# Kernel optimization log

Measured on AMD Instinct MI355X. Metric: run time of the kernel, lower is better.

Reference implementation:

```python
import jax, jax.numpy as jnp
import numpy as np

NUM_GRAPHS = 4096
NODES_PER_GRAPH = 24
EDGES_PER_GRAPH = 48
LG_EDGES_PER_GRAPH = 144
N_ITER = 4
HID = 128
IN_DIM = 70
EDGE_DIM = 6


def seg_softmax(v, seg, num_seg):
    # numerically-stable softmax over segments; v: [E,1]
    m = jax.ops.segment_max(v, seg, num_segments=num_seg)
    e = jnp.exp(v - m[seg])
    s = jax.ops.segment_sum(e, seg, num_segments=num_seg)
    return e / s[seg]


def setup_inputs() -> dict:
    key = jax.random.key(0)
    ks = jax.random.split(key, 20)
    B, NPG, EPG, LPG = NUM_GRAPHS, NODES_PER_GRAPH, EDGES_PER_GRAPH, LG_EDGES_PER_GRAPH
    N, E, LE = B * NPG, B * EPG, B * LPG
    # graph-consistent random connectivity
    goff_n = (jnp.arange(B, dtype=jnp.int32) * NPG)[:, None]
    src = (goff_n + jax.random.randint(ks[0], (B, EPG), 0, NPG)).reshape(-1)
    dst = (goff_n + jax.random.randint(ks[1], (B, EPG), 0, NPG)).reshape(-1)
    edge_index = jnp.stack([src, dst]).astype(jnp.int32)
    goff_e = (jnp.arange(B, dtype=jnp.int32) * EPG)[:, None]
    lsrc = (goff_e + jax.random.randint(ks[2], (B, LPG), 0, EPG)).reshape(-1)
    ldst = (goff_e + jax.random.randint(ks[3], (B, LPG), 0, EPG)).reshape(-1)
    lg_edge_index = jnp.stack([lsrc, ldst]).astype(jnp.int32)
    edge_batch = jnp.repeat(jnp.arange(B, dtype=jnp.int32), EPG)
    s = 0.1
    inp = {
        "x": jax.random.normal(ks[4], (N, IN_DIM), jnp.float32),
        "edge_attr": jax.random.normal(ks[5], (E, EDGE_DIM), jnp.float32),
        "edge_index": edge_index,
        "lg_edge_index": lg_edge_index,
        "edge_batch": edge_batch,
        # params (stored [in, out] so we apply x @ W + b)
        "w_mlp": jax.random.normal(ks[6], (IN_DIM, HID), jnp.float32) * s,
        "b_mlp": jnp.zeros((HID,), jnp.float32),
        "w_u": jax.random.normal(ks[7], (HID, HID), jnp.float32) * s,
        "w_v": jax.random.normal(ks[8], (HID, HID), jnp.float32) * s,
        "w_edge": jax.random.normal(ks[9], (EDGE_DIM, HID), jnp.float32) * s,
        "w_rel": jax.random.normal(ks[10], (HID, 1), jnp.float32) * s,
        "b_rel": jnp.zeros((1,), jnp.float32),
        "w_root": jax.random.normal(ks[11], (HID, 1), jnp.float32) * s,
        "a": jax.random.normal(ks[12], (1, HID, N_ITER), jnp.float32) * s,
        "a_bias": jnp.zeros((1, 1, N_ITER), jnp.float32),
        "w_gout": jax.random.normal(ks[13], (HID, HID), jnp.float32) * s,
        "b_gout": jnp.zeros((HID,), jnp.float32),
        "w_block": jax.random.normal(ks[14], (HID, HID), jnp.float32) * s,
        "b_block": jnp.zeros((HID,), jnp.float32),
    }
    return inp


def reference(x, edge_attr, edge_index, lg_edge_index, edge_batch,
              w_mlp, b_mlp, w_u, w_v, w_edge, w_rel, b_rel, w_root,
              a, a_bias, w_gout, b_gout, w_block, b_block):
    N = x.shape[0]
    src, dst = edge_index[0], edge_index[1]
    lsrc, ldst = lg_edge_index[0], lg_edge_index[1]
    E = src.shape[0]

    # DrugEncoder.mlp
    h = x @ w_mlp + b_mlp  # [N, H]

    # initial directed-edge features: (lin_u(x)[src] + lin_v(x)[dst] + lin_edge(e)) / 3
    e0 = (h @ w_u)[src] + (h @ w_v)[dst] + edge_attr @ w_edge
    e0 = e0 / 3.0  # [E, H]

    out = e0
    outs, gouts = [], []
    for _ in range(N_ITER):
        # line-graph message passing: scatter-add over line-graph edges
        out = e0 + jax.ops.segment_sum(out[lsrc], ldst, num_segments=E)
        # GlobalAttentionPool: GraphConv(H->1) on the line graph, segment softmax, weighted add-pool
        aggr = jax.ops.segment_sum(out[lsrc], ldst, num_segments=E)
        xc = aggr @ w_rel + b_rel + out @ w_root  # [E, 1]
        sc = seg_softmax(xc, edge_batch, NUM_GRAPHS)  # [E, 1]
        g = jax.ops.segment_sum(out * sc, edge_batch, num_segments=NUM_GRAPHS)  # [B, H]
        outs.append(out)
        gouts.append(jnp.tanh(g @ w_gout + b_gout))

    out_all = jnp.stack(outs, axis=-1)    # [E, H, T]
    gout_all = jnp.stack(gouts, axis=-1)  # [B, H, T]

    # temporal attention over iterations
    scores = jnp.einsum('bht,ht->bt', gout_all, a[0])[:, None, :] + a_bias  # [B,1,T]
    scores = jax.nn.softmax(scores, axis=-1)
    per_edge = scores[edge_batch]  # gather == repeat_interleave by per-graph edge counts
    out = (out_all * per_edge).sum(-1)  # [E, H]

    # scatter edge features back to destination nodes
    xo = h + jax.ops.segment_sum(out, dst, num_segments=N)
    xo = xo @ w_block + b_block  # LinearBlock.lin1
    return xo
```

## Files before the change

kernel.cpp:

```cpp
#include <hip/hip_runtime.h>

#define NGR 4096
#define NPG 24
#define EPG 48
#define LPG 144
#define NITER 4
#define HID 128
#define NN (NGR*NPG)
#define NE (NGR*EPG)
#define NL (NGR*LPG)

typedef unsigned int uint;
typedef unsigned short ushort;
typedef short bf16x8 __attribute__((ext_vector_type(8)));
typedef unsigned short u16x4 __attribute__((ext_vector_type(4)));
typedef float f32x4 __attribute__((ext_vector_type(4)));
typedef float f32x2 __attribute__((ext_vector_type(2)));

__device__ __forceinline__ float b2f(ushort u){ return __uint_as_float(((uint)u)<<16); }
__device__ __forceinline__ ushort f2b(float f){
  uint x = __float_as_uint(f);
  x += 0x7FFFu + ((x>>16)&1u);
  return (ushort)(x>>16);
}
__device__ __forceinline__ float wredsum(float v){
  #pragma unroll
  for(int m=32;m;m>>=1) v += __shfl_xor(v, m, 64);
  return v;
}
__device__ __forceinline__ f32x4 mfma16(bf16x8 a, bf16x8 b, f32x4 c){
  return __builtin_amdgcn_mfma_f32_16x16x32_bf16(a, b, c, 0, 0, 0);
}

__global__ __launch_bounds__(256) void k_prep(
    const float* __restrict__ wmlp, const float* __restrict__ wu,
    const float* __restrict__ wv, const float* __restrict__ wb,
    ushort* __restrict__ P)
{
  int id = blockIdx.x*256 + threadIdx.x;
  if(id < 12288){
    int n=id/96, k=id-n*96;
    float v=(k<70)? wmlp[k*128+n] : 0.f;
    ushort hb=f2b(v); P[id]=hb; P[12288+id]=f2b(v-b2f(hb));
  } else if(id < 28672){
    int i=id-12288, n=i>>7, k=i&127;
    float v=wu[k*128+n]; ushort hb=f2b(v);
    P[24576+i]=hb; P[40960+i]=f2b(v-b2f(hb));
  } else if(id < 45056){
    int i=id-28672, n=i>>7, k=i&127;
    float v=wv[k*128+n]; ushort hb=f2b(v);
    P[57344+i]=hb; P[73728+i]=f2b(v-b2f(hb));
  } else if(id < 61440){
    int i=id-45056, n=i>>7, k=i&127;
    float v=wb[k*128+n]; ushort hb=f2b(v);
    P[90112+i]=hb; P[106496+i]=f2b(v-b2f(hb));
  }
}

__global__ __launch_bounds__(256,3) void k_fused(
  const float* __restrict__ x, const float* __restrict__ ea,
  const int* __restrict__ eidx, const int* __restrict__ lidx,
  const ushort* __restrict__ P,
  const float* __restrict__ bmlp, const float* __restrict__ wedge,
  const float* __restrict__ wrel, const float* __restrict__ brel,
  const float* __restrict__ wroot,
  const float* __restrict__ aatt, const float* __restrict__ abias,
  const float* __restrict__ wgout, const float* __restrict__ bgout,
  const float* __restrict__ bblock,
  float* __restrict__ out)
{
  const int g=blockIdx.x, tid=threadIdx.x, lane=tid&63, wid=tid>>6;
  const int q=lane>>4, ln=lane&15;
  const int E0=g*EPG, L0=g*LPG;
  const int nA = wid*32 + ln;

  __shared__ __align__(16) char LB[48320];
  ushort* Hh   = (ushort*)(LB + 0);
  ushort* Hl   = (ushort*)(LB + 6528);
  ushort* A_bf = (ushort*)(LB + 13056);
  ushort* OUTh = (ushort*)(LB + 18432);
  ushort* OUTl = (ushort*)(LB + 30720);
  ushort* A_cnt= (ushort*)(LB + 18432);
  ushort* xh   = (ushort*)(LB + 18432);
  ushort* xl   = (ushort*)(LB + 24576);
  float*  Pe   = (float*) (LB + 30720);
  float*  Re   = (float*) (LB + 30912);
  float*  eaL  = (float*) (LB + 31104);
  float*  nacc = (float*) (LB + 18432);
  int*    esrc = (int*)   (LB + 43008);
  int*    edst = (int*)   (LB + 43200);
  float*  xcs  = (float*) (LB + 43392);
  float*  gsf  = (float*) (LB + 44160);
  float*  sfull= (float*) (LB + 46208);
  float*  score= (float*) (LB + 48256);
  float*  wts  = (float*) (LB + 48272);
  float*  zeroF= (float*) (LB + 48288);

  const ushort *WmH=P, *WmL=P+12288, *WuH=P+24576, *WuL=P+40960,
               *WvH=P+57344, *WvL=P+73728, *WbH=P+90112, *WbL=P+106496;
  const f32x4 z4 = {0.f,0.f,0.f,0.f};

  f32x2 gxa[4];
  const f32x2* xg2 = (const f32x2*)(x + (size_t)g*NPG*70);
  #pragma unroll
  for(int i=0;i<4;i++){ int idx=tid+256*i; if(idx<840) gxa[i]=xg2[idx]; }
  for(int idx=tid; idx<1536; idx+=256) ((uint*)A_cnt)[idx]=0u;
  if(tid<48){
    int s=eidx[E0+tid]-g*NPG, d=eidx[NE+E0+tid]-g*NPG;
    esrc[tid]=s; edst[tid]=d; Pe[tid]=0.f; Re[tid]=0.f;
  }
  if(tid<8) zeroF[tid]=0.f;
  for(int idx=tid; idx<288; idx+=256) eaL[idx]=ea[(size_t)E0*6+idx];
  for(int idx=tid; idx<512; idx+=256) sfull[idx]=0.f;
  __syncthreads();
  if(tid<LPG){ int ls=lidx[L0+tid]-E0, ld=lidx[NL+L0+tid]-E0;
    atomicAdd(((uint*)A_cnt) + ((ld*64+ls)>>1), 1u<<((ls&1)*16)); }
  __syncthreads();
  for(int idx=tid; idx<48*48; idx+=256){ int i=idx/48, j=idx-i*48;
    A_bf[i*56+j]=f2b((float)A_cnt[i*64+j]); }
  __syncthreads();
  #pragma unroll
  for(int i=0;i<4;i++){ int idx=tid+256*i; if(idx<840){
    int r=idx/35, c0=2*(idx-r*35);
    float v0=gxa[i].x, v1=gxa[i].y;
    ushort h0=f2b(v0), h1=f2b(v1);
    xh[r*96+c0]=h0;   xl[r*96+c0]=f2b(v0-b2f(h0));
    xh[r*96+c0+1]=h1; xl[r*96+c0+1]=f2b(v1-b2f(h1)); } }
  for(int idx=tid; idx<624; idx+=256){ int r=idx/26, c=70+(idx-r*26);
    xh[r*96+c]=0; xl[r*96+c]=0; }
  __syncthreads();

  {
    f32x4 hc[2][2];
    #pragma unroll
    for(int mt=0;mt<2;mt++){ hc[mt][0]=z4; hc[mt][1]=z4; }
    #pragma unroll
    for(int kt=0; kt<3; kt++){
      int ko=kt*32+q*8;
      bf16x8 ah0=*(const bf16x8*)&xh[ln*96+ko];
      bf16x8 ah1=*(const bf16x8*)&xh[(16+ln)*96+ko];
      bf16x8 al0=*(const bf16x8*)&xl[ln*96+ko];
      bf16x8 al1=*(const bf16x8*)&xl[(16+ln)*96+ko];
      #pragma unroll
      for(int nt=0;nt<2;nt++){
        int nb=(nA+nt*16)*96+ko;
        bf16x8 bh=*(const bf16x8*)&WmH[nb];
        bf16x8 bl=*(const bf16x8*)&WmL[nb];
        hc[0][nt]=mfma16(ah0,bh,hc[0][nt]);
        hc[0][nt]=mfma16(al0,bh,hc[0][nt]);
        hc[0][nt]=mfma16(ah0,bl,hc[0][nt]);
        hc[1][nt]=mfma16(ah1,bh,hc[1][nt]);
        hc[1][nt]=mfma16(al1,bh,hc[1][nt]);
        hc[1][nt]=mfma16(ah1,bl,hc[1][nt]);
      }
    }
    float bm0=bmlp[nA], bm1=bmlp[nA+16];
    #pragma unroll
    for(int nt=0;nt<2;nt++){ float bb=nt?bm1:bm0; int col=nA+nt*16;
      #pragma unroll
      for(int mt=0;mt<2;mt++)
        #pragma unroll
        for(int r=0;r<4;r++){
          int row=mt*16+q*4+r;
          if(row<24){
            float hvv=hc[mt][nt][r]+bb;
            ushort hb=f2b(hvv);
            Hh[row*136+col]=hb; Hl[row*136+col]=f2b(hvv-b2f(hb));
          }
        }
    }
  }
  __syncthreads();

  f32x4 e0f[3][2];
  {
    int sgm[3], dgm[3];
    #pragma unroll
    for(int mt=0;mt<3;mt++){ sgm[mt]=esrc[mt*16+ln]; dgm[mt]=edst[mt*16+ln]; }
    #pragma unroll
    for(int mt=0;mt<3;mt++){ e0f[mt][0]=z4; e0f[mt][1]=z4; }
    #pragma unroll
    for(int kt=0;kt<4;kt++){
      int ko=kt*32+q*8;
      bf16x8 BuH[2],BuL[2],BvH[2],BvL[2];
      #pragma unroll
      for(int nt=0;nt<2;nt++){
        int nb=(nA+nt*16)*128+ko;
        BuH[nt]=*(const bf16x8*)&WuH[nb]; BuL[nt]=*(const bf16x8*)&WuL[nb];
        BvH[nt]=*(const bf16x8*)&WvH[nb]; BvL[nt]=*(const bf16x8*)&WvL[nb];
      }
      #pragma unroll
      for(int mt=0;mt<3;mt++){
        bf16x8 ash=*(const bf16x8*)&Hh[sgm[mt]*136+ko];
        bf16x8 asl=*(const bf16x8*)&Hl[sgm[mt]*136+ko];
        bf16x8 adh=*(const bf16x8*)&Hh[dgm[mt]*136+ko];
        bf16x8 adl=*(const bf16x8*)&Hl[dgm[mt]*136+ko];
        #pragma unroll
        for(int nt=0;nt<2;nt++){
          f32x4 acc=e0f[mt][nt];
          acc=mfma16(ash,BuH[nt],acc);
          acc=mfma16(asl,BuH[nt],acc);
          acc=mfma16(ash,BuL[nt],acc);
          acc=mfma16(adh,BvH[nt],acc);
          acc=mfma16(adl,BvH[nt],acc);
          acc=mfma16(adh,BvL[nt],acc);
          e0f[mt][nt]=acc;
        }
      }
    }
  }
  {
    const float wrel0=wrel[nA], wrel1=wrel[nA+16];
    const float wroot0=wroot[nA], wroot1=wroot[nA+16];
    float wed0[6],wed1[6];
    #pragma unroll
    for(int k=0;k<6;k++){ wed0[k]=wedge[k*128+nA]; wed1[k]=wedge[k*128+nA+16]; }
    #pragma unroll
    for(int mt=0;mt<3;mt++)
      #pragma unroll
      for(int r=0;r<4;r++){
        int m=mt*16+q*4+r;
        float v0=e0f[mt][0][r], v1=e0f[mt][1][r];
        #pragma unroll
        for(int k=0;k<6;k++){ float e=eaL[m*6+k]; v0+=e*wed0[k]; v1+=e*wed1[k]; }
        e0f[mt][0][r]=v0*(1.f/3.f);
        e0f[mt][1][r]=v1*(1.f/3.f);
      }
    #pragma unroll
    for(int mt=0;mt<3;mt++)
      #pragma unroll
      for(int r=0;r<4;r++){
        float pp=e0f[mt][0][r]*wrel0  + e0f[mt][1][r]*wrel1;
        float rr=e0f[mt][0][r]*wroot0 + e0f[mt][1][r]*wroot1;
        #pragma unroll
        for(int msk=1;msk<16;msk<<=1){ pp+=__shfl_xor(pp,msk,64); rr+=__shfl_xor(rr,msk,64); }
        if(ln==0){ atomicAdd(&Pe[mt*16+q*4+r],pp); atomicAdd(&Re[mt*16+q*4+r],rr); }
      }
  }
  __syncthreads();

  if(wid==0){
    const float brel_f=brel[0];
    const int arow=(lane<48)?lane:0;
    float pprev=(lane<48)?Pe[lane]:0.f;
    float rprev=(lane<48)?Re[lane]:0.f;
    const float pe_l=pprev, re_l=rprev;
    float rlast=rprev;
    #pragma unroll
    for(int t=1;t<=5;t++){
      float s=0.f, sr=0.f;
      for(int j=0;j<48;j++){
        float a=b2f(A_bf[arow*56+j]);
        float pj=__shfl(pprev,j,64);
        float rj=__shfl(rprev,j,64);
        s+=a*pj; sr+=a*rj;
      }
      s+=pe_l; sr+=re_l;
      if(t>=2){
        float xv = s - pe_l + rlast + brel_f;
        float v=(lane<48)?xv:-3.0e38f;
        float mx=v;
        #pragma unroll
        for(int msk=32;msk;msk>>=1) mx=fmaxf(mx,__shfl_xor(mx,msk,64));
        float e2=(lane<48)?__expf(v-mx):0.f;
        float ss=e2;
        #pragma unroll
        for(int msk=32;msk;msk>>=1) ss+=__shfl_xor(ss,msk,64);
        if(lane<48) xcs[(t-2)*48+lane]=e2/ss;
      }
      pprev=s; rprev=sr; rlast=sr;
    }
  }
  __syncthreads();

  #define STORE_SPLIT(n_, mt_, v_) {                                        \
    int b_ = (mt_)*2 + (q>>1);                                              \
    int off_ = (n_)*48 + ((b_ ^ (((n_)>>3)&1))<<3) + ((q&1)<<2);            \
    u16x4 hh_, ll_;                                                         \
    _Pragma("unroll")                                                       \
    for(int r_=0;r_<4;r_++){ ushort h_=f2b((v_)[r_]);                       \
      hh_[r_]=h_; ll_[r_]=f2b((v_)[r_]-b2f(h_)); }                          \
    *(u16x4*)&OUTh[off_]=hh_; *(u16x4*)&OUTl[off_]=ll_; }

  f32x4 Ocur[3][2];
  #pragma unroll
  for(int mt=0;mt<3;mt++)
    #pragma unroll
    for(int nt=0;nt<2;nt++){
      int n=nA+nt*16;
      STORE_SPLIT(n, mt, e0f[mt][nt]);
    }
  #pragma unroll 1
  for(int t=0;t<NITER;t++){
    #pragma unroll
    for(int nt=0;nt<2;nt++){
      int n=nA+nt*16, sw=(n>>3)&1, base=n*48;
      bf16x8 Bh0=*(const bf16x8*)&OUTh[base+((q^sw)<<3)];
      bf16x8 Bl0=*(const bf16x8*)&OUTl[base+((q^sw)<<3)];
      const ushort* ph1=(q<2)? &OUTh[base+(((4+q)^sw)<<3)] : (const ushort*)zeroF;
      const ushort* pl1=(q<2)? &OUTl[base+(((4+q)^sw)<<3)] : (const ushort*)zeroF;
      bf16x8 Bh1=*(const bf16x8*)ph1;
      bf16x8 Bl1=*(const bf16x8*)pl1;
      #pragma unroll
      for(int mt=0;mt<3;mt++){
        int ar=(mt*16+ln)*56;
        bf16x8 a0=*(const bf16x8*)&A_bf[ar+q*8];
        const ushort* pa1=(q<2)? &A_bf[ar+32+q*8] : (const ushort*)zeroF;
        bf16x8 a1=*(const bf16x8*)pa1;
        f32x4 acc=e0f[mt][nt];
        acc=mfma16(a0,Bh0,acc);
        acc=mfma16(a1,Bh1,acc);
        acc=mfma16(a0,Bl0,acc);
        acc=mfma16(a1,Bl1,acc);
        Ocur[mt][nt]=acc;
      }
      #pragma unroll
      for(int mt=0;mt<3;mt++) STORE_SPLIT(n, mt, Ocur[mt][nt]);
    }
    float gp0=0.f, gp1=0.f;
    #pragma unroll
    for(int mt=0;mt<3;mt++)
      #pragma unroll
      for(int r=0;r<4;r++){
        float xcv=xcs[t*48+mt*16+q*4+r];
        gp0+=xcv*Ocur[mt][0][r];
        gp1+=xcv*Ocur[mt][1][r];
      }
    gp0+=__shfl_xor(gp0,16,64); gp0+=__shfl_xor(gp0,32,64);
    gp1+=__shfl_xor(gp1,16,64); gp1+=__shfl_xor(gp1,32,64);
    if(q==0){ gsf[t*128+nA]=gp0; gsf[t*128+nA+16]=gp1; }
  }
  __syncthreads();

  {
    float p00=0,p01=0,p10=0,p11=0,p20=0,p21=0,p30=0,p31=0;
    int k0=wid*32;
    for(int kk=0;kk<32;kk++){
      int k=k0+kk;
      f32x2 w=((const f32x2*)wgout)[k*64+lane];
      float g0=gsf[k], g1=gsf[128+k], g2=gsf[256+k], g3=gsf[384+k];
      p00+=g0*w.x; p01+=g0*w.y;
      p10+=g1*w.x; p11+=g1*w.y;
      p20+=g2*w.x; p21+=g2*w.y;
      p30+=g3*w.x; p31+=g3*w.y;
    }
    atomicAdd(&sfull[2*lane],p00);     atomicAdd(&sfull[2*lane+1],p01);
    atomicAdd(&sfull[128+2*lane],p10); atomicAdd(&sfull[128+2*lane+1],p11);
    atomicAdd(&sfull[256+2*lane],p20); atomicAdd(&sfull[256+2*lane+1],p21);
    atomicAdd(&sfull[384+2*lane],p30); atomicAdd(&sfull[384+2*lane+1],p31);
  }
  __syncthreads();
  {
    int t=wid;
    float s0v=sfull[t*128+2*lane]  +bgout[2*lane];
    float s1v=sfull[t*128+2*lane+1]+bgout[2*lane+1];
    float v=tanhf(s0v)*aatt[(2*lane)*4+t]+tanhf(s1v)*aatt[(2*lane+1)*4+t];
    v=wredsum(v);
    if(lane==0) score[t]=v+abias[t];
  }
  __syncthreads();
  if(tid==0){
    float m=fmaxf(fmaxf(score[0],score[1]),fmaxf(score[2],score[3]));
    float e0v=__expf(score[0]-m), e1v=__expf(score[1]-m),
          e2v=__expf(score[2]-m), e3v=__expf(score[3]-m);
    float s=e0v+e1v+e2v+e3v;
    wts[0]=e0v/s; wts[1]=e1v/s; wts[2]=e2v/s; wts[3]=e3v/s;
  }
  __syncthreads();

  {
    const float cc4=wts[3], cc3=cc4+wts[2], cc2=cc3+wts[1];
    f32x4 Z[3][2];
    #pragma unroll
    for(int mt=0;mt<3;mt++)
      #pragma unroll
      for(int nt=0;nt<2;nt++){
        #pragma unroll
        for(int r=0;r<4;r++) Z[mt][nt][r]=cc4*e0f[mt][nt][r];
        int n=nA+nt*16;
        STORE_SPLIT(n, mt, Z[mt][nt]);
      }
    #pragma unroll 1
    for(int s=0;s<NITER;s++){
      const float ci = (s==0)?cc3:(s==1)?cc2:1.f;
      #pragma unroll
      for(int nt=0;nt<2;nt++){
        int n=nA+nt*16, sw=(n>>3)&1, base=n*48;
        bf16x8 Bh0=*(const bf16x8*)&OUTh[base+((q^sw)<<3)];
        bf16x8 Bl0=*(const bf16x8*)&OUTl[base+((q^sw)<<3)];
        const ushort* ph1=(q<2)? &OUTh[base+(((4+q)^sw)<<3)] : (const ushort*)zeroF;
        const ushort* pl1=(q<2)? &OUTl[base+(((4+q)^sw)<<3)] : (const ushort*)zeroF;
        bf16x8 Bh1=*(const bf16x8*)ph1;
        bf16x8 Bl1=*(const bf16x8*)pl1;
        #pragma unroll
        for(int mt=0;mt<3;mt++){
          int ar=(mt*16+ln)*56;
          bf16x8 a0=*(const bf16x8*)&A_bf[ar+q*8];
          const ushort* pa1=(q<2)? &A_bf[ar+32+q*8] : (const ushort*)zeroF;
          bf16x8 a1=*(const bf16x8*)pa1;
          f32x4 acc;
          #pragma unroll
          for(int r=0;r<4;r++) acc[r]=ci*e0f[mt][nt][r];
          acc=mfma16(a0,Bh0,acc);
          acc=mfma16(a1,Bh1,acc);
          acc=mfma16(a0,Bl0,acc);
          acc=mfma16(a1,Bl1,acc);
          Z[mt][nt]=acc;
        }
        if(s<NITER-1){
          #pragma unroll
          for(int mt=0;mt<3;mt++) STORE_SPLIT(n, mt, Z[mt][nt]);
        }
      }
    }
    __syncthreads();
    for(int idx=tid; idx<3072; idx+=256) nacc[idx]=0.f;
    __syncthreads();
    #pragma unroll
    for(int mt=0;mt<3;mt++)
      #pragma unroll
      for(int nt=0;nt<2;nt++){
        int ncol=nA+nt*16;
        #pragma unroll
        for(int r=0;r<4;r++){
          int dn=edst[mt*16+q*4+r];
          atomicAdd(&nacc[dn*128+ncol],Z[mt][nt][r]);
        }
      }
  }
  __syncthreads();
  for(int idx=tid; idx<24*128; idx+=256){
    int n=idx>>7, k=idx&127;
    float zv=b2f(Hh[n*136+k])+b2f(Hl[n*136+k])+nacc[idx];
    ushort hb=f2b(zv);
    Hh[n*136+k]=hb; Hl[n*136+k]=f2b(zv-b2f(hb));
  }
  __syncthreads();
  {
    f32x4 c4[2][2];
    c4[0][0]=z4; c4[0][1]=z4; c4[1][0]=z4; c4[1][1]=z4;
    #pragma unroll
    for(int kt=0;kt<4;kt++){
      int ko=kt*32+q*8;
      bf16x8 ah0=*(const bf16x8*)&Hh[ln*136+ko];
      bf16x8 ah1=*(const bf16x8*)&Hh[(16+ln)*136+ko];
      bf16x8 al0=*(const bf16x8*)&Hl[ln*136+ko];
      bf16x8 al1=*(const bf16x8*)&Hl[(16+ln)*136+ko];
      #pragma unroll
      for(int nt=0;nt<2;nt++){
        int nb=(nA+nt*16)*128+ko;
        bf16x8 bh=*(const bf16x8*)&WbH[nb];
        bf16x8 bl=*(const bf16x8*)&WbL[nb];
        c4[0][nt]=mfma16(ah0,bh,c4[0][nt]);
        c4[0][nt]=mfma16(al0,bh,c4[0][nt]);
        c4[0][nt]=mfma16(ah0,bl,c4[0][nt]);
        c4[1][nt]=mfma16(ah1,bh,c4[1][nt]);
        c4[1][nt]=mfma16(al1,bh,c4[1][nt]);
        c4[1][nt]=mfma16(ah1,bl,c4[1][nt]);
      }
    }
    float bb0=bblock[nA], bb1=bblock[nA+16];
    #pragma unroll
    for(int nt=0;nt<2;nt++){ float bbx=nt?bb1:bb0; int col=nA+nt*16;
      #pragma unroll
      for(int mt=0;mt<2;mt++)
        #pragma unroll
        for(int r=0;r<4;r++){
          int row=mt*16+q*4+r;
          if(row<24) out[(size_t)(g*NPG+row)*128+col]=c4[mt][nt][r]+bbx;
        }
    }
  }
  #undef STORE_SPLIT
}

extern "C" void kernel_launch(void* const* d_in, const int* in_sizes, int n_in,
                              void* d_out, int out_size, void* d_ws, size_t ws_size,
                              hipStream_t stream)
{
  (void)in_sizes; (void)n_in; (void)out_size; (void)ws_size;
  const float* x      = (const float*)d_in[0];
  const float* eattr  = (const float*)d_in[1];
  const int*   eidx   = (const int*)d_in[2];
  const int*   lidx   = (const int*)d_in[3];
  const float* wmlp   = (const float*)d_in[5];
  const float* bmlp   = (const float*)d_in[6];
  const float* wu     = (const float*)d_in[7];
  const float* wvv    = (const float*)d_in[8];
  const float* wedge  = (const float*)d_in[9];
  const float* wrel   = (const float*)d_in[10];
  const float* brel   = (const float*)d_in[11];
  const float* wroot  = (const float*)d_in[12];
  const float* aatt   = (const float*)d_in[13];
  const float* abias  = (const float*)d_in[14];
  const float* wgout  = (const float*)d_in[15];
  const float* bgout  = (const float*)d_in[16];
  const float* wblock = (const float*)d_in[17];
  const float* bblock = (const float*)d_in[18];

  ushort* P = (ushort*)d_ws;

  k_prep <<<240, 256, 0, stream>>>(wmlp, wu, wvv, wblock, P);
  k_fused<<<NGR, 256, 0, stream>>>(x, eattr, eidx, lidx, P,
                                   bmlp, wedge, wrel, brel, wroot,
                                   aatt, abias, wgout, bgout, bblock,
                                   (float*)d_out);
}
```

Baseline: 548.8 us.

## Split each graph's work across eight waves instead of four

The fused per-graph kernel now launches 512 threads per block, so each wave owns a single 16-column output tile instead of two. The intent is more latency hiding and parallelism per graph, with fewer registers per thread. In exchange there are more waves per block, more barrier participants and more redundant A-matrix loads across waves. Launch bounds move from (256,3) to (512,4), which tightens the per-thread register budget.

Measured after the change: 739.4 us. 34.7% more time.

```diff
diff --git a/kernel.cpp b/kernel.cpp
--- a/kernel.cpp
+++ b/kernel.cpp
@@ -57,7 +57,7 @@
   }
 }
 
-__global__ __launch_bounds__(256,3) void k_fused(
+__global__ __launch_bounds__(512,4) void k_fused(
   const float* __restrict__ x, const float* __restrict__ ea,
   const int* __restrict__ eidx, const int* __restrict__ lidx,
   const ushort* __restrict__ P,
@@ -72,7 +72,7 @@
   const int g=blockIdx.x, tid=threadIdx.x, lane=tid&63, wid=tid>>6;
   const int q=lane>>4, ln=lane&15;
   const int E0=g*EPG, L0=g*LPG;
-  const int nA = wid*32 + ln;
+  const int nA = wid*16 + ln;
 
   __shared__ __align__(16) char LB[48320];
   ushort* Hh   = (ushort*)(LB + 0);
@@ -100,40 +100,39 @@
                *WvH=P+57344, *WvL=P+73728, *WbH=P+90112, *WbL=P+106496;
   const f32x4 z4 = {0.f,0.f,0.f,0.f};
 
-  f32x2 gxa[4];
+  f32x2 gxa[2];
   const f32x2* xg2 = (const f32x2*)(x + (size_t)g*NPG*70);
   #pragma unroll
-  for(int i=0;i<4;i++){ int idx=tid+256*i; if(idx<840) gxa[i]=xg2[idx]; }
-  for(int idx=tid; idx<1536; idx+=256) ((uint*)A_cnt)[idx]=0u;
+  for(int i=0;i<2;i++){ int idx=tid+512*i; if(idx<840) gxa[i]=xg2[idx]; }
+  for(int idx=tid; idx<1536; idx+=512) ((uint*)A_cnt)[idx]=0u;
   if(tid<48){
     int s=eidx[E0+tid]-g*NPG, d=eidx[NE+E0+tid]-g*NPG;
     esrc[tid]=s; edst[tid]=d; Pe[tid]=0.f; Re[tid]=0.f;
   }
   if(tid<8) zeroF[tid]=0.f;
-  for(int idx=tid; idx<288; idx+=256) eaL[idx]=ea[(size_t)E0*6+idx];
-  for(int idx=tid; idx<512; idx+=256) sfull[idx]=0.f;
+  if(tid<288) eaL[tid]=ea[(size_t)E0*6+tid];
+  if(tid<512) sfull[tid]=0.f;
   __syncthreads();
   if(tid<LPG){ int ls=lidx[L0+tid]-E0, ld=lidx[NL+L0+tid]-E0;
     atomicAdd(((uint*)A_cnt) + ((ld*64+ls)>>1), 1u<<((ls&1)*16)); }
   __syncthreads();
-  for(int idx=tid; idx<48*48; idx+=256){ int i=idx/48, j=idx-i*48;
+  for(int idx=tid; idx<48*48; idx+=512){ int i=idx/48, j=idx-i*48;
     A_bf[i*56+j]=f2b((float)A_cnt[i*64+j]); }
   __syncthreads();
   #pragma unroll
-  for(int i=0;i<4;i++){ int idx=tid+256*i; if(idx<840){
+  for(int i=0;i<2;i++){ int idx=tid+512*i; if(idx<840){
     int r=idx/35, c0=2*(idx-r*35);
     float v0=gxa[i].x, v1=gxa[i].y;
     ushort h0=f2b(v0), h1=f2b(v1);
     xh[r*96+c0]=h0;   xl[r*96+c0]=f2b(v0-b2f(h0));
     xh[r*96+c0+1]=h1; xl[r*96+c0+1]=f2b(v1-b2f(h1)); } }
-  for(int idx=tid; idx<624; idx+=256){ int r=idx/26, c=70+(idx-r*26);
+  for(int idx=tid; idx<624; idx+=512){ int r=idx/26, c=70+(idx-r*26);
     xh[r*96+c]=0; xl[r*96+c]=0; }
   __syncthreads();
 
   {
-    f32x4 hc[2][2];
-    #pragma unroll
-    for(int mt=0;mt<2;mt++){ hc[mt][0]=z4; hc[mt][1]=z4; }
+    f32x4 hc[2];
+    hc[0]=z4; hc[1]=z4;
     #pragma unroll
     for(int kt=0; kt<3; kt++){
       int ko=kt*32+q*8;
@@ -141,97 +140,83 @@
       bf16x8 ah1=*(const bf16x8*)&xh[(16+ln)*96+ko];
       bf16x8 al0=*(const bf16x8*)&xl[ln*96+ko];
       bf16x8 al1=*(const bf16x8*)&xl[(16+ln)*96+ko];
-      #pragma unroll
-      for(int nt=0;nt<2;nt++){
-        int nb=(nA+nt*16)*96+ko;
-        bf16x8 bh=*(const bf16x8*)&WmH[nb];
-        bf16x8 bl=*(const bf16x8*)&WmL[nb];
-        hc[0][nt]=mfma16(ah0,bh,hc[0][nt]);
-        hc[0][nt]=mfma16(al0,bh,hc[0][nt]);
-        hc[0][nt]=mfma16(ah0,bl,hc[0][nt]);
-        hc[1][nt]=mfma16(ah1,bh,hc[1][nt]);
-        hc[1][nt]=mfma16(al1,bh,hc[1][nt]);
-        hc[1][nt]=mfma16(ah1,bl,hc[1][nt]);
-      }
-    }
-    float bm0=bmlp[nA], bm1=bmlp[nA+16];
-    #pragma unroll
-    for(int nt=0;nt<2;nt++){ float bb=nt?bm1:bm0; int col=nA+nt*16;
-      #pragma unroll
-      for(int mt=0;mt<2;mt++)
-        #pragma unroll
-        for(int r=0;r<4;r++){
-          int row=mt*16+q*4+r;
-          if(row<24){
-            float hvv=hc[mt][nt][r]+bb;
-            ushort hb=f2b(hvv);
-            Hh[row*136+col]=hb; Hl[row*136+col]=f2b(hvv-b2f(hb));
-          }
+      int nb=nA*96+ko;
+      bf16x8 bh=*(const bf16x8*)&WmH[nb];
+      bf16x8 bl=*(const bf16x8*)&WmL[nb];
+      hc[0]=mfma16(ah0,bh,hc[0]);
+      hc[0]=mfma16(al0,bh,hc[0]);
+      hc[0]=mfma16(ah0,bl,hc[0]);
+      hc[1]=mfma16(ah1,bh,hc[1]);
+      hc[1]=mfma16(al1,bh,hc[1]);
+      hc[1]=mfma16(ah1,bl,hc[1]);
+    }
+    float bb=bmlp[nA];
+    #pragma unroll
+    for(int mt=0;mt<2;mt++)
+      #pragma unroll
+      for(int r=0;r<4;r++){
+        int row=mt*16+q*4+r;
+        if(row<24){
+          float hvv=hc[mt][r]+bb;
+          ushort hb=f2b(hvv);
+          Hh[row*136+nA]=hb; Hl[row*136+nA]=f2b(hvv-b2f(hb));
         }
-    }
-  }
-  __syncthreads();
-
-  f32x4 e0f[3][2];
+      }
+  }
+  __syncthreads();
+
+  f32x4 e0f[3];
   {
     int sgm[3], dgm[3];
     #pragma unroll
     for(int mt=0;mt<3;mt++){ sgm[mt]=esrc[mt*16+ln]; dgm[mt]=edst[mt*16+ln]; }
     #pragma unroll
-    for(int mt=0;mt<3;mt++){ e0f[mt][0]=z4; e0f[mt][1]=z4; }
+    for(int mt=0;mt<3;mt++) e0f[mt]=z4;
     #pragma unroll
     for(int kt=0;kt<4;kt++){
       int ko=kt*32+q*8;
-      bf16x8 BuH[2],BuL[2],BvH[2],BvL[2];
-      #pragma unroll
-      for(int nt=0;nt<2;nt++){
-        int nb=(nA+nt*16)*128+ko;
-        BuH[nt]=*(const bf16x8*)&WuH[nb]; BuL[nt]=*(const bf16x8*)&WuL[nb];
-        BvH[nt]=*(const bf16x8*)&WvH[nb]; BvL[nt]=*(const bf16x8*)&WvL[nb];
-      }
+      int nb=nA*128+ko;
+      bf16x8 BuH=*(const bf16x8*)&WuH[nb], BuL=*(const bf16x8*)&WuL[nb];
+      bf16x8 BvH=*(const bf16x8*)&WvH[nb], BvL=*(const bf16x8*)&WvL[nb];
       #pragma unroll
       for(int mt=0;mt<3;mt++){
         bf16x8 ash=*(const bf16x8*)&Hh[sgm[mt]*136+ko];
         bf16x8 asl=*(const bf16x8*)&Hl[sgm[mt]*136+ko];
         bf16x8 adh=*(const bf16x8*)&Hh[dgm[mt]*136+ko];
         bf16x8 adl=*(const bf16x8*)&Hl[dgm[mt]*136+ko];
-        #pragma unroll
-        for(int nt=0;nt<2;nt++){
-          f32x4 acc=e0f[mt][nt];
-          acc=mfma16(ash,BuH[nt],acc);
-          acc=mfma16(asl,BuH[nt],acc);
-          acc=mfma16(ash,BuL[nt],acc);
-          acc=mfma16(adh,BvH[nt],acc);
-          acc=mfma16(adl,BvH[nt],acc);
-          acc=mfma16(adh,BvL[nt],acc);
-          e0f[mt][nt]=acc;
-        }
-      }
-    }
-  }
-  {
-    const float wrel0=wrel[nA], wrel1=wrel[nA+16];
-    const float wroot0=wroot[nA], wroot1=wroot[nA+16];
-    float wed0[6],wed1[6];
-    #pragma unroll
-    for(int k=0;k<6;k++){ wed0[k]=wedge[k*128+nA]; wed1[k]=wedge[k*128+nA+16]; }
+        f32x4 acc=e0f[mt];
+        acc=mfma16(ash,BuH,acc);
+        acc=mfma16(asl,BuH,acc);
+        acc=mfma16(ash,BuL,acc);
+        acc=mfma16(adh,BvH,acc);
+        acc=mfma16(adl,BvH,acc);
+        acc=mfma16(adh,BvL,acc);
+        e0f[mt]=acc;
+      }
+    }
+  }
+  {
+    const float wrel0=wrel[nA];
+    const float wroot0=wroot[nA];
+    float wed0[6];
+    #pragma unroll
+    for(int k=0;k<6;k++) wed0[k]=wedge[k*128+nA];
     #pragma unroll
     for(int mt=0;mt<3;mt++)
       #pragma unroll
       for(int r=0;r<4;r++){
         int m=mt*16+q*4+r;
-        float v0=e0f[mt][0][r], v1=e0f[mt][1][r];
-        #pragma unroll
-        for(int k=0;k<6;k++){ float e=eaL[m*6+k]; v0+=e*wed0[k]; v1+=e*wed1[k]; }
-        e0f[mt][0][r]=v0*(1.f/3.f);
-        e0f[mt][1][r]=v1*(1.f/3.f);
+        float v0=e0f[mt][r];
+        #pragma unroll
+        for(int k=0;k<6;k++) v0+=eaL[m*6+k]*wed0[k];
+        e0f[mt][r]=v0*(1.f/3.f);
       }
     #pragma unroll
     for(int mt=0;mt<3;mt++)
       #pragma unroll
       for(int r=0;r<4;r++){
-        float pp=e0f[mt][0][r]*wrel0  + e0f[mt][1][r]*wrel1;
-        float rr=e0f[mt][0][r]*wroot0 + e0f[mt][1][r]*wroot1;
+        float pp=e0f[mt][r]*wrel0;
+        float rr=e0f[mt][r]*wroot0;
         #pragma unroll
         for(int msk=1;msk<16;msk<<=1){ pp+=__shfl_xor(pp,msk,64); rr+=__shfl_xor(rr,msk,64); }
         if(ln==0){ atomicAdd(&Pe[mt*16+q*4+r],pp); atomicAdd(&Re[mt*16+q*4+r],rr); }
@@ -282,60 +267,48 @@
       hh_[r_]=h_; ll_[r_]=f2b((v_)[r_]-b2f(h_)); }                          \
     *(u16x4*)&OUTh[off_]=hh_; *(u16x4*)&OUTl[off_]=ll_; }
 
-  f32x4 Ocur[3][2];
+  f32x4 Ocur[3];
   #pragma unroll
-  for(int mt=0;mt<3;mt++)
-    #pragma unroll
-    for(int nt=0;nt<2;nt++){
-      int n=nA+nt*16;
-      STORE_SPLIT(n, mt, e0f[mt][nt]);
-    }
+  for(int mt=0;mt<3;mt++) STORE_SPLIT(nA, mt, e0f[mt]);
+  const int swA=(nA>>3)&1, baseA=nA*48;
   #pragma unroll 1
   for(int t=0;t<NITER;t++){
-    #pragma unroll
-    for(int nt=0;nt<2;nt++){
-      int n=nA+nt*16, sw=(n>>3)&1, base=n*48;
-      bf16x8 Bh0=*(const bf16x8*)&OUTh[base+((q^sw)<<3)];
-      bf16x8 Bl0=*(const bf16x8*)&OUTl[base+((q^sw)<<3)];
-      const ushort* ph1=(q<2)? &OUTh[base+(((4+q)^sw)<<3)] : (const ushort*)zeroF;
-      const ushort* pl1=(q<2)? &OUTl[base+(((4+q)^sw)<<3)] : (const ushort*)zeroF;
-      bf16x8 Bh1=*(const bf16x8*)ph1;
-      bf16x8 Bl1=*(const bf16x8*)pl1;
-      #pragma unroll
-      for(int mt=0;mt<3;mt++){
-        int ar=(mt*16+ln)*56;
-        bf16x8 a0=*(const bf16x8*)&A_bf[ar+q*8];
-        const ushort* pa1=(q<2)? &A_bf[ar+32+q*8] : (const ushort*)zeroF;
-        bf16x8 a1=*(const bf16x8*)pa1;
-        f32x4 acc=e0f[mt][nt];
-        acc=mfma16(a0,Bh0,acc);
-        acc=mfma16(a1,Bh1,acc);
-        acc=mfma16(a0,Bl0,acc);
-        acc=mfma16(a1,Bl1,acc);
-        Ocur[mt][nt]=acc;
-      }
-      #pragma unroll
-      for(int mt=0;mt<3;mt++) STORE_SPLIT(n, mt, Ocur[mt][nt]);
-    }
-    float gp0=0.f, gp1=0.f;
+    bf16x8 Bh0=*(const bf16x8*)&OUTh[baseA+((q^swA)<<3)];
+    bf16x8 Bl0=*(const bf16x8*)&OUTl[baseA+((q^swA)<<3)];
+    const ushort* ph1=(q<2)? &OUTh[baseA+(((4+q)^swA)<<3)] : (const ushort*)zeroF;
+    const ushort* pl1=(q<2)? &OUTl[baseA+(((4+q)^swA)<<3)] : (const ushort*)zeroF;
+    bf16x8 Bh1=*(const bf16x8*)ph1;
+    bf16x8 Bl1=*(const bf16x8*)pl1;
+    #pragma unroll
+    for(int mt=0;mt<3;mt++){
+      int ar=(mt*16+ln)*56;
+      bf16x8 a0=*(const bf16x8*)&A_bf[ar+q*8];
+      const ushort* pa1=(q<2)? &A_bf[ar+32+q*8] : (const ushort*)zeroF;
+      bf16x8 a1=*(const bf16x8*)pa1;
+      f32x4 acc=e0f[mt];
+      acc=mfma16(a0,Bh0,acc);
+      acc=mfma16(a1,Bh1,acc);
+      acc=mfma16(a0,Bl0,acc);
+      acc=mfma16(a1,Bl1,acc);
+      Ocur[mt]=acc;
+    }
+    #pragma unroll
+    for(int mt=0;mt<3;mt++) STORE_SPLIT(nA, mt, Ocur[mt]);
+    float gp0=0.f;
     #pragma unroll
     for(int mt=0;mt<3;mt++)
       #pragma unroll
-      for(int r=0;r<4;r++){
-        float xcv=xcs[t*48+mt*16+q*4+r];
-        gp0+=xcv*Ocur[mt][0][r];
-        gp1+=xcv*Ocur[mt][1][r];
-      }
+      for(int r=0;r<4;r++)
+        gp0+=xcs[t*48+mt*16+q*4+r]*Ocur[mt][r];
     gp0+=__shfl_xor(gp0,16,64); gp0+=__shfl_xor(gp0,32,64);
-    gp1+=__shfl_xor(gp1,16,64); gp1+=__shfl_xor(gp1,32,64);
-    if(q==0){ gsf[t*128+nA]=gp0; gsf[t*128+nA+16]=gp1; }
+    if(q==0) gsf[t*128+nA]=gp0;
   }
   __syncthreads();
 
   {
     float p00=0,p01=0,p10=0,p11=0,p20=0,p21=0,p30=0,p31=0;
-    int k0=wid*32;
-    for(int kk=0;kk<32;kk++){
+    int k0=wid*16;
+    for(int kk=0;kk<16;kk++){
       int k=k0+kk;
       f32x2 w=((const f32x2*)wgout)[k*64+lane];
       float g0=gsf[k], g1=gsf[128+k], g2=gsf[256+k], g3=gsf[384+k];
@@ -350,7 +323,7 @@
     atomicAdd(&sfull[384+2*lane],p30); atomicAdd(&sfull[384+2*lane+1],p31);
   }
   __syncthreads();
-  {
+  if(wid<4){
     int t=wid;
     float s0v=sfull[t*128+2*lane]  +bgout[2*lane];
     float s1v=sfull[t*128+2*lane+1]+bgout[2*lane+1];
@@ -370,66 +343,55 @@
 
   {
     const float cc4=wts[3], cc3=cc4+wts[2], cc2=cc3+wts[1];
-    f32x4 Z[3][2];
-    #pragma unroll
-    for(int mt=0;mt<3;mt++)
-      #pragma unroll
-      for(int nt=0;nt<2;nt++){
-        #pragma unroll
-        for(int r=0;r<4;r++) Z[mt][nt][r]=cc4*e0f[mt][nt][r];
-        int n=nA+nt*16;
-        STORE_SPLIT(n, mt, Z[mt][nt]);
-      }
+    f32x4 Z[3];
+    #pragma unroll
+    for(int mt=0;mt<3;mt++){
+      #pragma unroll
+      for(int r=0;r<4;r++) Z[mt][r]=cc4*e0f[mt][r];
+      STORE_SPLIT(nA, mt, Z[mt]);
+    }
     #pragma unroll 1
     for(int s=0;s<NITER;s++){
       const float ci = (s==0)?cc3:(s==1)?cc2:1.f;
-      #pragma unroll
-      for(int nt=0;nt<2;nt++){
-        int n=nA+nt*16, sw=(n>>3)&1, base=n*48;
-        bf16x8 Bh0=*(const bf16x8*)&OUTh[base+((q^sw)<<3)];
-        bf16x8 Bl0=*(const bf16x8*)&OUTl[base+((q^sw)<<3)];
-        const ushort* ph1=(q<2)? &OUTh[base+(((4+q)^sw)<<3)] : (const ushort*)zeroF;
-        const ushort* pl1=(q<2)? &OUTl[base+(((4+q)^sw)<<3)] : (const ushort*)zeroF;
-        bf16x8 Bh1=*(const bf16x8*)ph1;
-        bf16x8 Bl1=*(const bf16x8*)pl1;
-        #pragma unroll
-        for(int mt=0;mt<3;mt++){
-          int ar=(mt*16+ln)*56;
-          bf16x8 a0=*(const bf16x8*)&A_bf[ar+q*8];
-          const ushort* pa1=(q<2)? &A_bf[ar+32+q*8] : (const ushort*)zeroF;
-          bf16x8 a1=*(const bf16x8*)pa1;
-          f32x4 acc;
-          #pragma unroll
-          for(int r=0;r<4;r++) acc[r]=ci*e0f[mt][nt][r];
-          acc=mfma16(a0,Bh0,acc);
-          acc=mfma16(a1,Bh1,acc);
-          acc=mfma16(a0,Bl0,acc);
-          acc=mfma16(a1,Bl1,acc);
-          Z[mt][nt]=acc;
-        }
-        if(s<NITER-1){
-          #pragma unroll
-          for(int mt=0;mt<3;mt++) STORE_SPLIT(n, mt, Z[mt][nt]);
-        }
+      bf16x8 Bh0=*(const bf16x8*)&OUTh[baseA+((q^swA)<<3)];
+      bf16x8 Bl0=*(const bf16x8*)&OUTl[baseA+((q^swA)<<3)];
+      const ushort* ph1=(q<2)? &OUTh[baseA+(((4+q)^swA)<<3)] : (const ushort*)zeroF;
+      const ushort* pl1=(q<2)? &OUTl[baseA+(((4+q)^swA)<<3)] : (const ushort*)zeroF;
+      bf16x8 Bh1=*(const bf16x8*)ph1;
+      bf16x8 Bl1=*(const bf16x8*)pl1;
+      #pragma unroll
+      for(int mt=0;mt<3;mt++){
+        int ar=(mt*16+ln)*56;
+        bf16x8 a0=*(const bf16x8*)&A_bf[ar+q*8];
+        const ushort* pa1=(q<2)? &A_bf[ar+32+q*8] : (const ushort*)zeroF;
+        bf16x8 a1=*(const bf16x8*)pa1;
+        f32x4 acc;
+        #pragma unroll
+        for(int r=0;r<4;r++) acc[r]=ci*e0f[mt][r];
+        acc=mfma16(a0,Bh0,acc);
+        acc=mfma16(a1,Bh1,acc);
+        acc=mfma16(a0,Bl0,acc);
+        acc=mfma16(a1,Bl1,acc);
+        Z[mt]=acc;
+      }
+      if(s<NITER-1){
+        #pragma unroll
+        for(int mt=0;mt<3;mt++) STORE_SPLIT(nA, mt, Z[mt]);
       }
     }
     __syncthreads();
-    for(int idx=tid; idx<3072; idx+=256) nacc[idx]=0.f;
+    for(int idx=tid; idx<3072; idx+=512) nacc[idx]=0.f;
     __syncthreads();
     #pragma unroll
     for(int mt=0;mt<3;mt++)
       #pragma unroll
-      for(int nt=0;nt<2;nt++){
-        int ncol=nA+nt*16;
-        #pragma unroll
-        for(int r=0;r<4;r++){
-          int dn=edst[mt*16+q*4+r];
-          atomicAdd(&nacc[dn*128+ncol],Z[mt][nt][r]);
-        }
-      }
-  }
-  __syncthreads();
-  for(int idx=tid; idx<24*128; idx+=256){
+      for(int r=0;r<4;r++){
+        int dn=edst[mt*16+q*4+r];
+        atomicAdd(&nacc[dn*128+nA],Z[mt][r]);
+      }
+  }
+  __syncthreads();
+  for(int idx=tid; idx<24*128; idx+=512){
     int n=idx>>7, k=idx&127;
     float zv=b2f(Hh[n*136+k])+b2f(Hl[n*136+k])+nacc[idx];
     ushort hb=f2b(zv);
@@ -437,8 +399,8 @@
   }
   __syncthreads();
   {
-    f32x4 c4[2][2];
-    c4[0][0]=z4; c4[0][1]=z4; c4[1][0]=z4; c4[1][1]=z4;
+    f32x4 c4[2];
+    c4[0]=z4; c4[1]=z4;
     #pragma unroll
     for(int kt=0;kt<4;kt++){
       int ko=kt*32+q*8;
@@ -446,30 +408,24 @@
       bf16x8 ah1=*(const bf16x8*)&Hh[(16+ln)*136+ko];
       bf16x8 al0=*(const bf16x8*)&Hl[ln*136+ko];
       bf16x8 al1=*(const bf16x8*)&Hl[(16+ln)*136+ko];
-      #pragma unroll
-      for(int nt=0;nt<2;nt++){
-        int nb=(nA+nt*16)*128+ko;
-        bf16x8 bh=*(const bf16x8*)&WbH[nb];
-        bf16x8 bl=*(const bf16x8*)&WbL[nb];
-        c4[0][nt]=mfma16(ah0,bh,c4[0][nt]);
-        c4[0][nt]=mfma16(al0,bh,c4[0][nt]);
-        c4[0][nt]=mfma16(ah0,bl,c4[0][nt]);
-        c4[1][nt]=mfma16(ah1,bh,c4[1][nt]);
-        c4[1][nt]=mfma16(al1,bh,c4[1][nt]);
-        c4[1][nt]=mfma16(ah1,bl,c4[1][nt]);
-      }
-    }
-    float bb0=bblock[nA], bb1=bblock[nA+16];
-    #pragma unroll
-    for(int nt=0;nt<2;nt++){ float bbx=nt?bb1:bb0; int col=nA+nt*16;
-      #pragma unroll
-      for(int mt=0;mt<2;mt++)
-        #pragma unroll
-        for(int r=0;r<4;r++){
-          int row=mt*16+q*4+r;
-          if(row<24) out[(size_t)(g*NPG+row)*128+col]=c4[mt][nt][r]+bbx;
-        }
-    }
+      int nb=nA*128+ko;
+      bf16x8 bh=*(const bf16x8*)&WbH[nb];
+      bf16x8 bl=*(const bf16x8*)&WbL[nb];
+      c4[0]=mfma16(ah0,bh,c4[0]);
+      c4[0]=mfma16(al0,bh,c4[0]);
+      c4[0]=mfma16(ah0,bl,c4[0]);
+      c4[1]=mfma16(ah1,bh,c4[1]);
+      c4[1]=mfma16(al1,bh,c4[1]);
+      c4[1]=mfma16(ah1,bl,c4[1]);
+    }
+    float bbx=bblock[nA];
+    #pragma unroll
+    for(int mt=0;mt<2;mt++)
+      #pragma unroll
+      for(int r=0;r<4;r++){
+        int row=mt*16+q*4+r;
+        if(row<24) out[(size_t)(g*NPG+row)*128+nA]=c4[mt][r]+bbx;
+      }
   }
   #undef STORE_SPLIT
 }
@@ -501,7 +457,7 @@
   ushort* P = (ushort*)d_ws;
 
   k_prep <<<240, 256, 0, stream>>>(wmlp, wu, wvv, wblock, P);
-  k_fused<<<NGR, 256, 0, stream>>>(x, eattr, eidx, lidx, P,
+  k_fused<<<NGR, 512, 0, stream>>>(x, eattr, eidx, lidx, P,
                                    bmlp, wedge, wrel, brel, wroot,
                                    aatt, abias, wgout, bgout, bblock,
                                    (float*)d_out);
```
